# Performance work log

Hardware: AMD Instinct MI355X
Metric: run time of the kernel (lower is better)

The kernel has to match this reference:

```python
import jax, jax.numpy as jnp
import numpy as np

LAMBDA_ATTENTION = 0.33
LAMBDA_DISTANCE = 0.33
LAMBDA_ADJACENCY = 1.0 - LAMBDA_ATTENTION - LAMBDA_DISTANCE
EPS = 1e-06
NEG_INF = 1000000000000.0


def setup_inputs() -> dict:
    key = jax.random.key(0)
    kq, kk, kv, ka, kd = jax.random.split(key, 5)
    B, H, S, D = 16, 16, 512, 64
    return {
        "query": jax.random.normal(kq, (B, H, S, D), dtype=jnp.float32),
        "key": jax.random.normal(kk, (B, H, S, D), dtype=jnp.float32),
        "value": jax.random.normal(kv, (B, H, S, D), dtype=jnp.float32),
        "mask": jnp.ones((B, 1, S), dtype=jnp.float32),
        "adj_matrix": jax.random.uniform(ka, (B, S, S), dtype=jnp.float32),
        "distance_matrix": jax.random.uniform(kd, (B, S, S), dtype=jnp.float32),
    }


def reference(query, key, value, mask, adj_matrix, distance_matrix):
    d_k = query.shape[-1]
    # scores: [B,H,S,S]
    scores = jnp.einsum("bhqd,bhkd->bhqk", query, key) / jnp.sqrt(jnp.asarray(d_k, query.dtype))
    # mask [B,1,S] -> broadcast to [B,H,S,S] over key axis
    key_mask = mask[:, :, None, :]  # [B,1,1,S]
    scores = jnp.where(key_mask == 0, -NEG_INF, scores)
    p_attn = jax.nn.softmax(scores, axis=-1)

    # row-normalized adjacency, broadcast over heads
    adj_norm = adj_matrix / (jnp.sum(adj_matrix, axis=-1, keepdims=True) + EPS)  # [B,S,S]

    # distance kernel: mask key positions with +inf then softmax(-x)
    dist = jnp.where(mask == 0, jnp.inf, distance_matrix)  # mask [B,1,S] broadcasts over rows
    p_dist = jax.nn.softmax(-dist, axis=-1)  # [B,S,S]

    p_weighted = (LAMBDA_ATTENTION * p_attn
                  + LAMBDA_DISTANCE * p_dist[:, None, :, :]
                  + LAMBDA_ADJACENCY * adj_norm[:, None, :, :])
    # dropout is identity in eval mode
    out = jnp.einsum("bhqk,bhkd->bhqd", p_weighted, value)
    return out, p_attn
```

## Files before the change

### kernel.cpp

```cpp
#include <hip/hip_runtime.h>
#include <cmath>

#define BATCH 16
#define HEADS 16
#define SEQ   512
#define DIM   64

#define LAMBDA_A 0.33f
#define LAMBDA_D 0.33f
#define LAMBDA_J 0.34f
#define NEG_BIG  1.0e12f

typedef float  floatx4 __attribute__((ext_vector_type(4)));
typedef short  shortx8 __attribute__((ext_vector_type(8)));
typedef short  shortx4 __attribute__((ext_vector_type(4)));

__device__ __forceinline__ unsigned short f2bf(float x){
  unsigned u = __builtin_bit_cast(unsigned, x);
  u += 0x7FFFu + ((u >> 16) & 1u);
  return (unsigned short)(u >> 16);
}

__global__ __launch_bounds__(256, 8) void prep_kernel(
    const float* __restrict__ adj, const float* __restrict__ dist,
    const float* __restrict__ mask, const float* __restrict__ K,
    const float* __restrict__ V, float* __restrict__ W,
    unsigned short* __restrict__ Kb, unsigned short* __restrict__ VTb)
{
  __shared__ unsigned short sT[64 * 72];
  int tid = threadIdx.x;

  if (blockIdx.x < BATCH * SEQ / 4){
    int lane = tid & 63;
    int row  = blockIdx.x * 4 + (tid >> 6);
    int b = row >> 9, q = row & (SEQ - 1);
    const float* arow = adj  + ((size_t)b * SEQ + q) * SEQ;
    const float* drow = dist + ((size_t)b * SEQ + q) * SEQ;
    const float* mrow = mask + (size_t)b * SEQ;

    floatx4 a[2], e[2];
    float asum = 0.f, dsum = 0.f;
#pragma unroll
    for (int i = 0; i < 2; i++){
      int c4 = (i * 64 + lane) * 4;
      a[i] = *(const floatx4*)(arow + c4);
      floatx4 d4 = *(const floatx4*)(drow + c4);
      floatx4 m4 = *(const floatx4*)(mrow + c4);
#pragma unroll
      for (int j = 0; j < 4; j++){
        asum += a[i][j];
        float ex = (m4[j] == 0.f) ? 0.f : __expf(-d4[j]);
        e[i][j] = ex;
        dsum += ex;
      }
    }
#pragma unroll
    for (int off = 1; off < 64; off <<= 1){
      asum += __shfl_xor(asum, off);
      dsum += __shfl_xor(dsum, off);
    }
    float ia = LAMBDA_J / (asum + 1e-6f);
    float id = LAMBDA_D / dsum;

    float* wrow = W + ((size_t)b * SEQ + q) * SEQ;
#pragma unroll
    for (int i = 0; i < 2; i++){
      int c4 = (i * 64 + lane) * 4;
      floatx4 w;
#pragma unroll
      for (int j = 0; j < 4; j++) w[j] = e[i][j] * id + a[i][j] * ia;
      *(floatx4*)(wrow + c4) = w;
    }
    return;
  }

  int bid = blockIdx.x - BATCH * SEQ / 4;
  int c   = bid & 7;
  int bh  = bid >> 3;
  const float* Kp = K + ((size_t)bh * SEQ + c * 64) * DIM;
  const float* Vp = V + ((size_t)bh * SEQ + c * 64) * DIM;
  unsigned short* Ko = Kb  + ((size_t)bh * SEQ + c * 64) * DIM;
  unsigned short* Vo = VTb + (size_t)bh * DIM * SEQ;

#pragma unroll
  for (int i = 0; i < 2; i++){
    int idx = (i * 256 + tid) * 8;
    floatx4 v0 = *(const floatx4*)(Kp + idx);
    floatx4 v1 = *(const floatx4*)(Kp + idx + 4);
    shortx8 hh;
#pragma unroll
    for (int j = 0; j < 4; j++){
      hh[j]     = (short)f2bf(v0[j]);
      hh[j + 4] = (short)f2bf(v1[j]);
    }
    *(shortx8*)(Ko + idx) = hh;
  }

#pragma unroll
  for (int i = 0; i < 4; i++){
    int idx = (i * 256 + tid) * 4;
    int k = idx >> 6, d = idx & 63;
    floatx4 v = *(const floatx4*)(Vp + idx);
#pragma unroll
    for (int j = 0; j < 4; j++) sT[(d + j) * 72 + k] = f2bf(v[j]);
  }
  __syncthreads();
#pragma unroll
  for (int i = 0; i < 2; i++){
    int idx = i * 256 + tid;
    int d = idx >> 3, k8 = idx & 7;
    shortx8 hh = *(const shortx8*)&sT[d * 72 + k8 * 8];
    *(shortx8*)(Vo + (size_t)d * SEQ + c * 64 + k8 * 8) = hh;
  }
}

__global__ __launch_bounds__(256, 2) void attn_kernel(
    const float* __restrict__ Q, const unsigned short* __restrict__ Kb,
    const unsigned short* __restrict__ VTb, const float* __restrict__ mask,
    const float* __restrict__ W, float* __restrict__ out, float* __restrict__ pattn)
{
  int bx = blockIdx.x;
  int qt = bx & 7;
  int h  = (bx >> 3) & 15;
  int b  = bx >> 7;
  int bh = b * HEADS + h;

  int tid  = threadIdx.x;
  int wv   = tid >> 6;
  int lane = tid & 63;
  int l15  = lane & 15;
  int quad = lane >> 4;
  int q0   = qt * 64 + wv * 16;

  __shared__ short sPW[4][16 * 72];
  short* slab = &sPW[wv][0];

  const float* Qp = Q + ((size_t)bh * SEQ + q0 + l15) * DIM + quad * 8;
  shortx8 qf[2];
#pragma unroll
  for (int ks = 0; ks < 2; ks++){
    floatx4 v0 = *(const floatx4*)(Qp + ks * 32);
    floatx4 v1 = *(const floatx4*)(Qp + ks * 32 + 4);
#pragma unroll
    for (int j = 0; j < 4; j++){
      qf[ks][j]     = (short)f2bf(v0[j] * 0.125f);
      qf[ks][j + 4] = (short)f2bf(v1[j] * 0.125f);
    }
  }

  const unsigned short* Kw = Kb + (size_t)bh * SEQ * DIM
                                + (size_t)l15 * DIM + quad * 8;
  floatx4 acc[32];
#pragma unroll
  for (int j = 0; j < 32; j++) acc[j] = (floatx4)0.f;
#pragma unroll
  for (int j = 0; j < 32; j++){
    const unsigned short* Kt = Kw + (size_t)j * 16 * DIM;
    shortx8 k0 = *(const shortx8*)(Kt);
    shortx8 k1 = *(const shortx8*)(Kt + 32);
    acc[j] = __builtin_amdgcn_mfma_f32_16x16x32_bf16(k0, qf[0], acc[j], 0, 0, 0);
    acc[j] = __builtin_amdgcn_mfma_f32_16x16x32_bf16(k1, qf[1], acc[j], 0, 0, 0);
  }

  const float* mrow = mask + b * SEQ + quad * 4;
  float mx = -INFINITY;
#pragma unroll
  for (int j = 0; j < 32; j++){
    floatx4 m4 = *(const floatx4*)(mrow + j * 16);
#pragma unroll
    for (int r = 0; r < 4; r++){
      float s = (m4[r] == 0.f) ? -NEG_BIG : acc[j][r];
      acc[j][r] = s;
      mx = fmaxf(mx, s);
    }
  }
  mx = fmaxf(mx, __shfl_xor(mx, 16));
  mx = fmaxf(mx, __shfl_xor(mx, 32));

  float sm = 0.f;
#pragma unroll
  for (int j = 0; j < 32; j++){
#pragma unroll
    for (int r = 0; r < 4; r++){
      float e = __expf(acc[j][r] - mx);
      acc[j][r] = e;
      sm += e;
    }
  }
  sm += __shfl_xor(sm, 16);
  sm += __shfl_xor(sm, 32);
  float inv_l  = 1.f / sm;
  float lam_il = LAMBDA_A * inv_l;

  float* pAl = pattn + ((size_t)bh * SEQ + q0 + l15) * SEQ + quad * 4;
  const float* Wl = W + ((size_t)b * SEQ + q0 + l15) * SEQ + quad * 4;
  const unsigned short* Vw = VTb + (size_t)bh * DIM * SEQ
                                 + (size_t)l15 * SEQ + quad * 8;

  floatx4 acc2[4];
#pragma unroll
  for (int d = 0; d < 4; d++) acc2[d] = (floatx4)0.f;

  floatx4 wcur[4], wnxt[4];
#pragma unroll
  for (int jj = 0; jj < 4; jj++) wcur[jj] = *(const floatx4*)(Wl + jj * 16);

#pragma unroll
  for (int cc = 0; cc < 8; cc++){
    if (cc < 7){
#pragma unroll
      for (int jj = 0; jj < 4; jj++)
        wnxt[jj] = *(const floatx4*)(Wl + (cc + 1) * 64 + jj * 16);
    }
#pragma unroll
    for (int jj = 0; jj < 4; jj++){
      int j = cc * 4 + jj;
      floatx4 pa;
      shortx4 pw;
#pragma unroll
      for (int r = 0; r < 4; r++){
        float e = acc[j][r];
        pa[r] = e * inv_l;
        pw[r] = (short)f2bf(fmaf(e, lam_il, wcur[jj][r]));
      }
      __builtin_nontemporal_store(pa, (floatx4*)(pAl + j * 16));
      *(shortx4*)&slab[l15 * 72 + jj * 16 + quad * 4] = pw;
    }
    const unsigned short* Vc = Vw + cc * 64;
#pragma unroll
    for (int ks = 0; ks < 2; ks++){
      shortx8 a2 = *(const shortx8*)&slab[l15 * 72 + ks * 32 + quad * 8];
#pragma unroll
      for (int d = 0; d < 4; d++){
        shortx8 vf = *(const shortx8*)(Vc + (size_t)d * 16 * SEQ + ks * 32);
        acc2[d] = __builtin_amdgcn_mfma_f32_16x16x32_bf16(a2, vf, acc2[d], 0, 0, 0);
      }
    }
#pragma unroll
    for (int jj = 0; jj < 4; jj++) wcur[jj] = wnxt[jj];
  }

  float* ob = out + ((size_t)bh * SEQ + q0 + quad * 4) * DIM + l15;
#pragma unroll
  for (int d = 0; d < 4; d++){
#pragma unroll
    for (int r = 0; r < 4; r++)
      __builtin_nontemporal_store(acc2[d][r], ob + (size_t)r * DIM + d * 16);
  }
}

extern "C" void kernel_launch(void* const* d_in, const int* in_sizes, int n_in,
                              void* d_out, int out_size, void* d_ws, size_t ws_size,
                              hipStream_t stream){
  const float* Q    = (const float*)d_in[0];
  const float* K    = (const float*)d_in[1];
  const float* V    = (const float*)d_in[2];
  const float* mask = (const float*)d_in[3];
  const float* adj  = (const float*)d_in[4];
  const float* dist = (const float*)d_in[5];
  float* out   = (float*)d_out;
  float* pattn = out + (size_t)BATCH * HEADS * SEQ * DIM;

  float*          Wbuf = (float*)d_ws;
  unsigned short* Kb   = (unsigned short*)((char*)d_ws + (size_t)16 * 1024 * 1024);
  unsigned short* VTb  = (unsigned short*)((char*)d_ws + (size_t)32 * 1024 * 1024);

  prep_kernel<<<BATCH * SEQ / 4 + BATCH * HEADS * 8, 256, 0, stream>>>(
      adj, dist, mask, K, V, Wbuf, Kb, VTb);
  attn_kernel<<<BATCH * HEADS * (SEQ / 64), 256, 0, stream>>>(
      Q, Kb, VTb, mask, Wbuf, out, pattn);
}
```

Measured before the change: 547.4 us.

## Recompute QK^T in second pass with online softmax to cut register use

```diff
diff --git a/kernel.cpp b/kernel.cpp
--- a/kernel.cpp
+++ b/kernel.cpp
@@ -114,7 +114,7 @@
   }
 }
 
-__global__ __launch_bounds__(256, 2) void attn_kernel(
+__global__ __launch_bounds__(256, 4) void attn_kernel(
     const float* __restrict__ Q, const unsigned short* __restrict__ Kb,
     const unsigned short* __restrict__ VTb, const float* __restrict__ mask,
     const float* __restrict__ W, float* __restrict__ out, float* __restrict__ pattn)
@@ -150,46 +150,38 @@
 
   const unsigned short* Kw = Kb + (size_t)bh * SEQ * DIM
                                 + (size_t)l15 * DIM + quad * 8;
-  floatx4 acc[32];
-#pragma unroll
-  for (int j = 0; j < 32; j++) acc[j] = (floatx4)0.f;
+  const float* mrow = mask + b * SEQ + quad * 4;
+
+  float mx = -INFINITY, lsum = 0.f;
 #pragma unroll
   for (int j = 0; j < 32; j++){
     const unsigned short* Kt = Kw + (size_t)j * 16 * DIM;
     shortx8 k0 = *(const shortx8*)(Kt);
     shortx8 k1 = *(const shortx8*)(Kt + 32);
-    acc[j] = __builtin_amdgcn_mfma_f32_16x16x32_bf16(k0, qf[0], acc[j], 0, 0, 0);
-    acc[j] = __builtin_amdgcn_mfma_f32_16x16x32_bf16(k1, qf[1], acc[j], 0, 0, 0);
-  }
-
-  const float* mrow = mask + b * SEQ + quad * 4;
-  float mx = -INFINITY;
-#pragma unroll
-  for (int j = 0; j < 32; j++){
+    floatx4 t = (floatx4)0.f;
+    t = __builtin_amdgcn_mfma_f32_16x16x32_bf16(k0, qf[0], t, 0, 0, 0);
+    t = __builtin_amdgcn_mfma_f32_16x16x32_bf16(k1, qf[1], t, 0, 0, 0);
     floatx4 m4 = *(const floatx4*)(mrow + j * 16);
-#pragma unroll
-    for (int r = 0; r < 4; r++){
-      float s = (m4[r] == 0.f) ? -NEG_BIG : acc[j][r];
-      acc[j][r] = s;
-      mx = fmaxf(mx, s);
-    }
-  }
-  mx = fmaxf(mx, __shfl_xor(mx, 16));
-  mx = fmaxf(mx, __shfl_xor(mx, 32));
-
-  float sm = 0.f;
-#pragma unroll
-  for (int j = 0; j < 32; j++){
-#pragma unroll
-    for (int r = 0; r < 4; r++){
-      float e = __expf(acc[j][r] - mx);
-      acc[j][r] = e;
-      sm += e;
-    }
-  }
-  sm += __shfl_xor(sm, 16);
-  sm += __shfl_xor(sm, 32);
-  float inv_l  = 1.f / sm;
+    float s0 = (m4[0] == 0.f) ? -NEG_BIG : t[0];
+    float s1 = (m4[1] == 0.f) ? -NEG_BIG : t[1];
+    float s2 = (m4[2] == 0.f) ? -NEG_BIG : t[2];
+    float s3 = (m4[3] == 0.f) ? -NEG_BIG : t[3];
+    float tm = fmaxf(fmaxf(s0, s1), fmaxf(s2, s3));
+    float mn = fmaxf(mx, tm);
+    lsum = lsum * __expf(mx - mn)
+         + __expf(s0 - mn) + __expf(s1 - mn)
+         + __expf(s2 - mn) + __expf(s3 - mn);
+    mx = mn;
+  }
+#pragma unroll
+  for (int off = 16; off < 64; off <<= 1){
+    float m2 = __shfl_xor(mx, off);
+    float l2 = __shfl_xor(lsum, off);
+    float mn = fmaxf(mx, m2);
+    lsum = lsum * __expf(mx - mn) + l2 * __expf(m2 - mn);
+    mx = mn;
+  }
+  float inv_l  = 1.f / lsum;
   float lam_il = LAMBDA_A * inv_l;
 
   float* pAl = pattn + ((size_t)bh * SEQ + q0 + l15) * SEQ + quad * 4;
@@ -201,31 +193,36 @@
 #pragma unroll
   for (int d = 0; d < 4; d++) acc2[d] = (floatx4)0.f;
 
-  floatx4 wcur[4], wnxt[4];
-#pragma unroll
-  for (int jj = 0; jj < 4; jj++) wcur[jj] = *(const floatx4*)(Wl + jj * 16);
-
 #pragma unroll
   for (int cc = 0; cc < 8; cc++){
-    if (cc < 7){
-#pragma unroll
-      for (int jj = 0; jj < 4; jj++)
-        wnxt[jj] = *(const floatx4*)(Wl + (cc + 1) * 64 + jj * 16);
-    }
+    floatx4 wc[4];
+#pragma unroll
+    for (int jj = 0; jj < 4; jj++)
+      wc[jj] = *(const floatx4*)(Wl + cc * 64 + jj * 16);
+
 #pragma unroll
     for (int jj = 0; jj < 4; jj++){
       int j = cc * 4 + jj;
+      const unsigned short* Kt = Kw + (size_t)j * 16 * DIM;
+      shortx8 k0 = *(const shortx8*)(Kt);
+      shortx8 k1 = *(const shortx8*)(Kt + 32);
+      floatx4 t = (floatx4)0.f;
+      t = __builtin_amdgcn_mfma_f32_16x16x32_bf16(k0, qf[0], t, 0, 0, 0);
+      t = __builtin_amdgcn_mfma_f32_16x16x32_bf16(k1, qf[1], t, 0, 0, 0);
+      floatx4 m4 = *(const floatx4*)(mrow + j * 16);
       floatx4 pa;
       shortx4 pw;
 #pragma unroll
       for (int r = 0; r < 4; r++){
-        float e = acc[j][r];
+        float s = (m4[r] == 0.f) ? -NEG_BIG : t[r];
+        float e = __expf(s - mx);
         pa[r] = e * inv_l;
-        pw[r] = (short)f2bf(fmaf(e, lam_il, wcur[jj][r]));
+        pw[r] = (short)f2bf(fmaf(e, lam_il, wc[jj][r]));
       }
       __builtin_nontemporal_store(pa, (floatx4*)(pAl + j * 16));
       *(shortx4*)&slab[l15 * 72 + jj * 16 + quad * 4] = pw;
     }
+
     const unsigned short* Vc = Vw + cc * 64;
 #pragma unroll
     for (int ks = 0; ks < 2; ks++){
@@ -236,8 +233,6 @@
         acc2[d] = __builtin_amdgcn_mfma_f32_16x16x32_bf16(a2, vf, acc2[d], 0, 0, 0);
       }
     }
-#pragma unroll
-    for (int jj = 0; jj < 4; jj++) wcur[jj] = wnxt[jj];
   }
 
   float* ob = out + ((size_t)bh * SEQ + q0 + quad * 4) * DIM + l15;
```

Result: slower. 587.9 us (+7.4%).

## Split key range across wave pairs to halve per-wave registers and raise occupancy

Applied to the files above, without the earlier changes.

```diff
diff --git a/kernel.cpp b/kernel.cpp
--- a/kernel.cpp
+++ b/kernel.cpp
@@ -114,28 +114,33 @@
   }
 }
 
-__global__ __launch_bounds__(256, 2) void attn_kernel(
+__global__ __launch_bounds__(256, 4) void attn_kernel(
     const float* __restrict__ Q, const unsigned short* __restrict__ Kb,
     const unsigned short* __restrict__ VTb, const float* __restrict__ mask,
     const float* __restrict__ W, float* __restrict__ out, float* __restrict__ pattn)
 {
   int bx = blockIdx.x;
-  int qt = bx & 7;
-  int h  = (bx >> 3) & 15;
-  int b  = bx >> 7;
+  int qt = bx & 15;
+  int h  = (bx >> 4) & 15;
+  int b  = bx >> 8;
   int bh = b * HEADS + h;
+  int q0b = qt * 32;
 
   int tid  = threadIdx.x;
   int wv   = tid >> 6;
   int lane = tid & 63;
   int l15  = lane & 15;
   int quad = lane >> 4;
-  int q0   = qt * 64 + wv * 16;
-
-  __shared__ short sPW[4][16 * 72];
+  int mt   = wv >> 1;
+  int p    = wv & 1;
+
+  __shared__ short   sPW[4][16 * 72];
+  __shared__ floatx4 sPart[2][64][5];
+  __shared__ float   sRedM[2][32];
+  __shared__ float   sRedS[2][32];
   short* slab = &sPW[wv][0];
 
-  const float* Qp = Q + ((size_t)bh * SEQ + q0 + l15) * DIM + quad * 8;
+  const float* Qp = Q + ((size_t)bh * SEQ + q0b + mt * 16 + l15) * DIM + quad * 8;
   shortx8 qf[2];
 #pragma unroll
   for (int ks = 0; ks < 2; ks++){
@@ -149,12 +154,12 @@
   }
 
   const unsigned short* Kw = Kb + (size_t)bh * SEQ * DIM
-                                + (size_t)l15 * DIM + quad * 8;
-  floatx4 acc[32];
-#pragma unroll
-  for (int j = 0; j < 32; j++) acc[j] = (floatx4)0.f;
-#pragma unroll
-  for (int j = 0; j < 32; j++){
+                                + (size_t)(p * 256 + l15) * DIM + quad * 8;
+  floatx4 acc[16];
+#pragma unroll
+  for (int j = 0; j < 16; j++) acc[j] = (floatx4)0.f;
+#pragma unroll
+  for (int j = 0; j < 16; j++){
     const unsigned short* Kt = Kw + (size_t)j * 16 * DIM;
     shortx8 k0 = *(const shortx8*)(Kt);
     shortx8 k1 = *(const shortx8*)(Kt + 32);
@@ -162,56 +167,67 @@
     acc[j] = __builtin_amdgcn_mfma_f32_16x16x32_bf16(k1, qf[1], acc[j], 0, 0, 0);
   }
 
-  const float* mrow = mask + b * SEQ + quad * 4;
-  float mx = -INFINITY;
-#pragma unroll
-  for (int j = 0; j < 32; j++){
+  const float* mrow = mask + b * SEQ + p * 256 + quad * 4;
+  float mx4[4] = {-INFINITY, -INFINITY, -INFINITY, -INFINITY};
+#pragma unroll
+  for (int j = 0; j < 16; j++){
     floatx4 m4 = *(const floatx4*)(mrow + j * 16);
 #pragma unroll
     for (int r = 0; r < 4; r++){
       float s = (m4[r] == 0.f) ? -NEG_BIG : acc[j][r];
       acc[j][r] = s;
-      mx = fmaxf(mx, s);
-    }
-  }
+      mx4[r] = fmaxf(mx4[r], s);
+    }
+  }
+  float mx = fmaxf(fmaxf(mx4[0], mx4[1]), fmaxf(mx4[2], mx4[3]));
   mx = fmaxf(mx, __shfl_xor(mx, 16));
   mx = fmaxf(mx, __shfl_xor(mx, 32));
 
-  float sm = 0.f;
-#pragma unroll
-  for (int j = 0; j < 32; j++){
+  float sm4[4] = {0.f, 0.f, 0.f, 0.f};
+#pragma unroll
+  for (int j = 0; j < 16; j++){
 #pragma unroll
     for (int r = 0; r < 4; r++){
       float e = __expf(acc[j][r] - mx);
       acc[j][r] = e;
-      sm += e;
-    }
-  }
+      sm4[r] += e;
+    }
+  }
+  float sm = (sm4[0] + sm4[1]) + (sm4[2] + sm4[3]);
   sm += __shfl_xor(sm, 16);
   sm += __shfl_xor(sm, 32);
-  float inv_l  = 1.f / sm;
+
+  if (lane < 16){
+    sRedM[p][mt * 16 + l15] = mx;
+    sRedS[p][mt * 16 + l15] = sm;
+  }
+  __syncthreads();
+  float m0 = sRedM[0][mt * 16 + l15], m1 = sRedM[1][mt * 16 + l15];
+  float l0 = sRedS[0][mt * 16 + l15], l1 = sRedS[1][mt * 16 + l15];
+  float mg = fmaxf(m0, m1);
+  float lg = l0 * __expf(m0 - mg) + l1 * __expf(m1 - mg);
+  float corr   = __expf(mx - mg);
+  float inv_l  = corr / lg;
   float lam_il = LAMBDA_A * inv_l;
 
-  float* pAl = pattn + ((size_t)bh * SEQ + q0 + l15) * SEQ + quad * 4;
-  const float* Wl = W + ((size_t)b * SEQ + q0 + l15) * SEQ + quad * 4;
+  float* pAl = pattn + ((size_t)bh * SEQ + q0b + mt * 16 + l15) * SEQ
+                     + p * 256 + quad * 4;
+  const float* Wl = W + ((size_t)b * SEQ + q0b + mt * 16 + l15) * SEQ
+                      + p * 256 + quad * 4;
   const unsigned short* Vw = VTb + (size_t)bh * DIM * SEQ
-                                 + (size_t)l15 * SEQ + quad * 8;
+                                 + (size_t)l15 * SEQ + p * 256 + quad * 8;
 
   floatx4 acc2[4];
 #pragma unroll
   for (int d = 0; d < 4; d++) acc2[d] = (floatx4)0.f;
 
-  floatx4 wcur[4], wnxt[4];
-#pragma unroll
-  for (int jj = 0; jj < 4; jj++) wcur[jj] = *(const floatx4*)(Wl + jj * 16);
-
-#pragma unroll
-  for (int cc = 0; cc < 8; cc++){
-    if (cc < 7){
-#pragma unroll
-      for (int jj = 0; jj < 4; jj++)
-        wnxt[jj] = *(const floatx4*)(Wl + (cc + 1) * 64 + jj * 16);
-    }
+#pragma unroll
+  for (int cc = 0; cc < 4; cc++){
+    floatx4 wc[4];
+#pragma unroll
+    for (int jj = 0; jj < 4; jj++)
+      wc[jj] = *(const floatx4*)(Wl + cc * 64 + jj * 16);
+
 #pragma unroll
     for (int jj = 0; jj < 4; jj++){
       int j = cc * 4 + jj;
@@ -221,11 +237,12 @@
       for (int r = 0; r < 4; r++){
         float e = acc[j][r];
         pa[r] = e * inv_l;
-        pw[r] = (short)f2bf(fmaf(e, lam_il, wcur[jj][r]));
+        pw[r] = (short)f2bf(fmaf(e, lam_il, wc[jj][r]));
       }
       __builtin_nontemporal_store(pa, (floatx4*)(pAl + j * 16));
       *(shortx4*)&slab[l15 * 72 + jj * 16 + quad * 4] = pw;
     }
+
     const unsigned short* Vc = Vw + cc * 64;
 #pragma unroll
     for (int ks = 0; ks < 2; ks++){
@@ -236,16 +253,22 @@
         acc2[d] = __builtin_amdgcn_mfma_f32_16x16x32_bf16(a2, vf, acc2[d], 0, 0, 0);
       }
     }
-#pragma unroll
-    for (int jj = 0; jj < 4; jj++) wcur[jj] = wnxt[jj];
-  }
-
-  float* ob = out + ((size_t)bh * SEQ + q0 + quad * 4) * DIM + l15;
-#pragma unroll
-  for (int d = 0; d < 4; d++){
-#pragma unroll
-    for (int r = 0; r < 4; r++)
-      __builtin_nontemporal_store(acc2[d][r], ob + (size_t)r * DIM + d * 16);
+  }
+
+  if (p == 1){
+#pragma unroll
+    for (int d = 0; d < 4; d++) sPart[mt][lane][d] = acc2[d];
+  }
+  __syncthreads();
+  if (p == 0){
+    float* ob = out + ((size_t)bh * SEQ + q0b + mt * 16 + quad * 4) * DIM + l15;
+#pragma unroll
+    for (int d = 0; d < 4; d++){
+      floatx4 o = acc2[d] + sPart[mt][lane][d];
+#pragma unroll
+      for (int r = 0; r < 4; r++)
+        __builtin_nontemporal_store(o[r], ob + (size_t)r * DIM + d * 16);
+    }
   }
 }
 
@@ -267,6 +290,6 @@
 
   prep_kernel<<<BATCH * SEQ / 4 + BATCH * HEADS * 8, 256, 0, stream>>>(
       adj, dist, mask, K, V, Wbuf, Kb, VTb);
-  attn_kernel<<<BATCH * HEADS * (SEQ / 64), 256, 0, stream>>>(
+  attn_kernel<<<BATCH * HEADS * (SEQ / 32), 256, 0, stream>>>(
       Q, Kb, VTb, mask, Wbuf, out, pattn);
 }
```

Measured after the change: 529.1 us. 3.4% less time.
